# Kernel optimization log

Hardware: AMD Instinct MI355X
Metric: run time of the kernel (lower is better)

## Reference

```python
import jax, jax.numpy as jnp
import numpy as np

B, S, H, NH = 1, 4096, 768, 12
D = H // NH  # per-head dim = 64


def setup_inputs() -> dict:
    key = jax.random.key(0)
    ks = jax.random.split(key, 10)
    p = 0.02  # param scale
    return {
        "x": jax.random.normal(ks[0], (B, S, H), jnp.float32),
        "Wq": jax.random.normal(ks[1], (H, H), jnp.float32) * p,
        "bq": jax.random.normal(ks[2], (H,), jnp.float32) * p,
        "Wk": jax.random.normal(ks[3], (H, H), jnp.float32) * p,
        "bk": jax.random.normal(ks[4], (H,), jnp.float32) * p,
        "Wv": jax.random.normal(ks[5], (H, H), jnp.float32) * p,
        "bv": jax.random.normal(ks[6], (H,), jnp.float32) * p,
        "Wo": jax.random.normal(ks[7], (H, H), jnp.float32) * p,
        "bo": jax.random.normal(ks[8], (H,), jnp.float32) * p,
        "attn_mask": jax.random.randint(ks[9], (B, 1, 1, S), 0, 2).astype(bool),
    }


def _split_heads(t):
    # [B, S, H] -> [B, NH, S, D]
    return t.reshape(B, S, NH, D).transpose(0, 2, 1, 3)


def reference(x, Wq, bq, Wk, bk, Wv, bv, Wo, bo, attn_mask):
    q = _split_heads(x @ Wq.T + bq)
    k = _split_heads(x @ Wk.T + bk)
    v = _split_heads(x @ Wv.T + bv)
    scores = jnp.einsum('bhqd,bhkd->bhqk', q, k) / np.sqrt(D).astype(np.float32)
    scores = jnp.where(attn_mask, jnp.float32(-1e9), scores)
    attn = jax.nn.softmax(scores, axis=-1)
    ctx = jnp.einsum('bhqk,bhkd->bhqd', attn, v)
    ctx = ctx.transpose(0, 2, 1, 3).reshape(B, S, H)  # merge heads
    return ctx @ Wo.T + bo
```

## Files before the change

kernel.cpp:

```cpp
#include <hip/hip_runtime.h>
#include <stdint.h>

#define S_LEN 4096
#define HDIM  768
#define NHEAD 12
#define DHEAD 64

typedef _Float16 f16;
typedef __attribute__((ext_vector_type(8)))  _Float16 f16x8;
typedef __attribute__((ext_vector_type(4)))  _Float16 f16x4;
typedef __attribute__((ext_vector_type(4)))  float    f32x4;
typedef __attribute__((ext_vector_type(16))) float    f32x16;

typedef __attribute__((address_space(1))) void gv_t;
typedef __attribute__((address_space(3))) void lv_t;

__device__ __forceinline__ void async_copy16(const void* g, void* l) {
  __builtin_amdgcn_global_load_lds((gv_t*)g, (lv_t*)l, 16, 0, 0);
}

__device__ __forceinline__ float fast_exp2(float x) {
#if __has_builtin(__builtin_amdgcn_exp2f)
  return __builtin_amdgcn_exp2f(x);
#else
  return exp2f(x);
#endif
}

__device__ __forceinline__ int swz4(int row) { return (row ^ (row >> 2)) & 3; }

constexpr size_t OFF_META = 0;
constexpr size_t OFF_RIDX = 256;
constexpr size_t OFF_XB   = 65536;
constexpr size_t SZ_XB    = (size_t)S_LEN * HDIM * 2;
constexpr size_t OFF_WQKV = OFF_XB + SZ_XB;
constexpr size_t SZ_WQKV  = (size_t)3 * HDIM * HDIM * 2;
constexpr size_t OFF_WO   = OFF_WQKV + SZ_WQKV;
constexpr size_t SZ_WO    = (size_t)HDIM * HDIM * 2;
constexpr size_t OFF_Q    = OFF_WO + SZ_WO;
constexpr size_t SZ_HD    = (size_t)NHEAD * S_LEN * DHEAD * 2;
constexpr size_t OFF_K    = OFF_Q + SZ_HD;
constexpr size_t OFF_VT   = OFF_K + SZ_HD;
constexpr size_t OFF_VR   = OFF_VT + SZ_HD;
constexpr size_t OFF_PO1  = OFF_VR + SZ_HD;

__global__ __launch_bounds__(256) void k_prep(const float* __restrict__ x,
                                              const float* __restrict__ wq,
                                              const float* __restrict__ wk,
                                              const float* __restrict__ wv,
                                              const float* __restrict__ wo,
                                              const int* __restrict__ mi,
                                              f16* __restrict__ dst,
                                              int* __restrict__ ridx,
                                              int* __restrict__ meta) {
  __shared__ int s_flag;
  __shared__ int s_cnt[256];
  const int b = blockIdx.x, tid = threadIdx.x;
  if (b < 5376) {
    int i = b * 256 + tid;
    const float* src; int off;
    if (i < 786432) { src = x; off = i; }
    else {
      int j = i - 786432;
      int w = j / 147456;
      off = j - w * 147456;
      src = (w == 0) ? wq : (w == 1) ? wk : (w == 2) ? wv : wo;
    }
    float4 v = ((const float4*)src)[off];
    f16x4 h;
    h[0] = (f16)v.x; h[1] = (f16)v.y; h[2] = (f16)v.z; h[3] = (f16)v.w;
    ((f16x4*)dst)[i] = h;
    return;
  }
  if (tid == 0) s_flag = 1;
  __syncthreads();
  int bad = 0;
  #pragma unroll
  for (int k = 0; k < 4; ++k) {
    int v = mi[k * 256 + tid];
    if (v != 0 && v != 1) bad = 1;
  }
  if (bad) atomicAnd(&s_flag, 0);
  __syncthreads();
  const int isInt = s_flag;
  const unsigned char* mu8 = (const unsigned char*)mi;
  int keep[16]; int cnt = 0;
  const int s0 = tid * 16;
  #pragma unroll
  for (int k = 0; k < 16; ++k) {
    int mval = isInt ? mi[s0 + k] : (int)mu8[s0 + k];
    keep[k] = (mval == 0) ? 1 : 0;
    cnt += keep[k];
    ridx[s0 + k] = 0;
  }
  s_cnt[tid] = cnt;
  __syncthreads();
  for (int off = 1; off < 256; off <<= 1) {
    int t = (tid >= off) ? s_cnt[tid - off] : 0;
    __syncthreads();
    s_cnt[tid] += t;
    __syncthreads();
  }
  int base = s_cnt[tid] - cnt;
  #pragma unroll
  for (int k = 0; k < 16; ++k) {
    if (keep[k]) { ridx[base] = s0 + k; ++base; }
  }
  if (tid == 255) meta[0] = s_cnt[255];
}

__global__ __launch_bounds__(256) void k_qkv(
    const f16* __restrict__ xb, const f16* __restrict__ wqkv,
    const float* __restrict__ bq, const float* __restrict__ bk, const float* __restrict__ bv,
    const int* __restrict__ ridx, const int* __restrict__ meta,
    f16* __restrict__ Qh, f16* __restrict__ Kc, f16* __restrict__ Vrow) {
  __shared__ __attribute__((aligned(16))) f16 lA[128 * 32];
  __shared__ __attribute__((aligned(16))) f16 lB[128 * 32];
  const int tid = threadIdx.x;
  const int wid = tid >> 6, lane = tid & 63;
  const int hf = lane >> 5, l31 = lane & 31;
  const int wm = wid >> 1, wn = wid & 1;
  const int tn = blockIdx.x;
  const int m0 = blockIdx.y * 128;
  const int mat = tn / 6;
  const int nb = (tn % 6) * 128;
  const int kc = meta[0];
  if (mat != 0 && m0 >= kc) return;
  const f16* wbase = wqkv + (size_t)mat * HDIM * HDIM;

  const int ar0 = tid >> 2, ar1 = 64 + (tid >> 2);
  const f16* asrc0;
  const f16* asrc1;
  if (mat == 0) {
    asrc0 = xb + (size_t)(m0 + ar0) * HDIM;
    asrc1 = xb + (size_t)(m0 + ar1) * HDIM;
  } else {
    int g0 = (m0 + ar0 < kc) ? ridx[m0 + ar0] : 0;
    int g1 = (m0 + ar1 < kc) ? ridx[m0 + ar1] : 0;
    asrc0 = xb + (size_t)g0 * HDIM;
    asrc1 = xb + (size_t)g1 * HDIM;
  }
  const int slot = tid & 3;
  const int gs0 = slot ^ swz4(ar0);
  const int gs1 = slot ^ swz4(ar1);

  f32x16 acc[2][2] = {};

  for (int k0 = 0; k0 < HDIM; k0 += 32) {
    async_copy16((const char*)(asrc0 + k0) + gs0 * 16, (char*)lA + (wid * 64) * 16);
    async_copy16((const char*)(asrc1 + k0) + gs1 * 16, (char*)lA + (256 + wid * 64) * 16);
    async_copy16((const char*)(wbase + (size_t)(nb + ar0) * HDIM + k0) + gs0 * 16,
                 (char*)lB + (wid * 64) * 16);
    async_copy16((const char*)(wbase + (size_t)(nb + ar1) * HDIM + k0) + gs1 * 16,
                 (char*)lB + (256 + wid * 64) * 16);
    __syncthreads();
    #pragma unroll
    for (int kk = 0; kk < 2; ++kk) {
      f16x8 af[2], bf[2];
      #pragma unroll
      for (int mi = 0; mi < 2; ++mi) {
        int row = wm * 64 + mi * 32 + l31;
        af[mi] = *(const f16x8*)&lA[row * 32 + (((kk * 2 + hf) ^ swz4(row)) * 8)];
      }
      #pragma unroll
      for (int ni = 0; ni < 2; ++ni) {
        int row = wn * 64 + ni * 32 + l31;
        bf[ni] = *(const f16x8*)&lB[row * 32 + (((kk * 2 + hf) ^ swz4(row)) * 8)];
      }
      #pragma unroll
      for (int mi = 0; mi < 2; ++mi)
        #pragma unroll
        for (int ni = 0; ni < 2; ++ni)
          acc[mi][ni] = __builtin_amdgcn_mfma_f32_32x32x16_f16(af[mi], bf[ni], acc[mi][ni], 0, 0, 0);
    }
    __syncthreads();
  }

  const float* bias = (mat == 0) ? bq : (mat == 1) ? bk : bv;
  const float qscale = 0.125f * 1.44269504088896341f;
  f16* kvdst = (mat == 1) ? Kc : Vrow;
  #pragma unroll
  for (int mi = 0; mi < 2; ++mi) {
    #pragma unroll
    for (int ni = 0; ni < 2; ++ni) {
      int n = nb + wn * 64 + ni * 32 + l31;
      int head = n >> 6, d = n & 63;
      float b = bias[n];
      #pragma unroll
      for (int reg = 0; reg < 16; ++reg) {
        int s = m0 + wm * 64 + mi * 32 + (reg & 3) + 8 * (reg >> 2) + 4 * hf;
        float val = acc[mi][ni][reg] + b;
        if (mat == 0) {
          Qh[((size_t)head * S_LEN + s) * DHEAD + d] = (f16)(val * qscale);
        } else if (s < kc) {
          kvdst[((size_t)head * S_LEN + s) * DHEAD + d] = (f16)val;
        }
      }
    }
  }
}

__global__ __launch_bounds__(256) void k_vt(const int* __restrict__ meta,
                                            const f16* __restrict__ Vrow,
                                            f16* __restrict__ Vtc,
                                            f16* __restrict__ Kc) {
  const int kc = meta[0];
  const int kcp = (kc + 63) & ~63;
  const int p0 = blockIdx.x * 64;
  const int h = blockIdx.y;
  const int tid = threadIdx.x;
  if (p0 >= kcp) return;
  if (p0 <= kc && kc < p0 + 64 && kc < kcp) {
    const int npad = kcp - kc;
    for (int u = tid; u < npad * 8; u += 256) {
      int r = kc + (u >> 3), c8 = u & 7;
      f16x8 z = {};
      *(f16x8*)&Kc[((size_t)h * S_LEN + r) * DHEAD + c8 * 8] = z;
    }
  }
  __shared__ __attribute__((aligned(16))) f16 lT[64 * 80];
  for (int u = tid; u < 512; u += 256) {
    int d8 = u >> 6, p = u & 63;
    f16x8 v = {};
    if (p0 + p < kc) v = *(const f16x8*)&Vrow[((size_t)h * S_LEN + p0 + p) * DHEAD + d8 * 8];
    #pragma unroll
    for (int j = 0; j < 8; ++j) lT[(d8 * 8 + j) * 80 + p] = v[j];
  }
  __syncthreads();
  for (int w = tid; w < 512; w += 256) {
    int d = w >> 3, p8 = w & 7;
    int base16 = (p8 >> 1) * 16, half = p8 & 1;
    f16x4 lo = *(const f16x4*)&lT[d * 80 + base16 + half * 4];
    f16x4 hi = *(const f16x4*)&lT[d * 80 + base16 + 8 + half * 4];
    f16x8 o;
    o[0] = lo[0]; o[1] = lo[1]; o[2] = lo[2]; o[3] = lo[3];
    o[4] = hi[0]; o[5] = hi[1]; o[6] = hi[2]; o[7] = hi[3];
    *(f16x8*)&Vtc[((size_t)h * DHEAD + d) * S_LEN + p0 + p8 * 8] = o;
  }
}

__global__ __launch_bounds__(256, 3) void k_attn(
    const f16* __restrict__ Qh, const f16* __restrict__ Kc, const f16* __restrict__ Vtc,
    const int* __restrict__ meta, f16* __restrict__ PO0, f16* __restrict__ PO1,
    float* __restrict__ PL) {
  __shared__ __attribute__((aligned(16))) f16 lK[2][64 * 64];
  __shared__ __attribute__((aligned(16))) f16 lV[2][64 * 64];
  const int tid = threadIdx.x;
  const int wid = tid >> 6, lane = tid & 63;
  const int hf = lane >> 5, l31 = lane & 31, r7 = l31 & 7;

  const int lid = blockIdx.x;
  const int w = ((lid & 7) * 96) + (lid >> 3);
  const int head = w >> 6;
  const int rem = w & 63;
  const int split = rem >> 5;
  const int q0 = (rem & 31) * 128 + wid * 32;

  const int kc = meta[0];
  const int nkt = (kc + 63) >> 6;
  const int th = nkt >> 1;
  const int t0 = split ? th : 0;
  const int t1 = split ? nkt : th;

  const f16* Qp = Qh + ((size_t)head * S_LEN + q0 + l31) * DHEAD;
  f16x8 qf[4];
  #pragma unroll
  for (int dc = 0; dc < 4; ++dc) qf[dc] = *(const f16x8*)(Qp + dc * 16 + hf * 8);

  f32x16 accO[2] = {};
  float ls0 = 0.f, ls1 = 0.f, ls2 = 0.f, ls3 = 0.f;

  const char* kbase = (const char*)(Kc + (size_t)head * S_LEN * DHEAD);
  const char* vbase = (const char*)(Vtc + (size_t)head * DHEAD * S_LEN);

  const int c0row = tid >> 3,         c0slot = tid & 7;
  const int c1row = (256 + tid) >> 3, c1slot = tid & 7;
  const int gs0 = c0slot ^ (c0row & 7);
  const int gs1 = c1slot ^ (c1row & 7);

  auto stage = [&](int t, int buf) {
    const int j0 = t * 64;
    async_copy16(kbase + (size_t)(j0 + c0row) * 128 + gs0 * 16,
                 (char*)&lK[buf][0] + (wid * 64) * 16);
    async_copy16(vbase + (size_t)c0row * (S_LEN * 2) + (size_t)j0 * 2 + gs0 * 16,
                 (char*)&lV[buf][0] + (wid * 64) * 16);
    async_copy16(kbase + (size_t)(j0 + c1row) * 128 + gs1 * 16,
                 (char*)&lK[buf][0] + (256 + wid * 64) * 16);
    async_copy16(vbase + (size_t)c1row * (S_LEN * 2) + (size_t)j0 * 2 + gs1 * 16,
                 (char*)&lV[buf][0] + (256 + wid * 64) * 16);
  };

  int cur = 0;
  if (t0 < t1) {
    stage(t0, 0);
    __syncthreads();
  }

  for (int t = t0; t < t1; ++t) {
    const bool more = (t + 1 < t1);
    if (more) stage(t + 1, cur ^ 1);

    #pragma unroll
    for (int mh = 0; mh < 2; ++mh) {
      f16x8 af[4];
      const int arow = mh * 32 + l31;
      #pragma unroll
      for (int dc = 0; dc < 4; ++dc)
        af[dc] = *(const f16x8*)&lK[cur][arow * 64 + ((((dc << 1) | hf) ^ r7) * 8)];
      f32x16 s = {};
      #pragma unroll
      for (int dc = 0; dc < 4; ++dc)
        s = __builtin_amdgcn_mfma_f32_32x32x16_f16(af[dc], qf[dc], s, 0, 0, 0);
      #pragma unroll
      for (int u = 0; u < 16; ++u) {
        s[u] = fast_exp2(s[u]);
        if ((u & 3) == 0) ls0 += s[u];
        else if ((u & 3) == 1) ls1 += s[u];
        else if ((u & 3) == 2) ls2 += s[u];
        else ls3 += s[u];
      }
      #pragma unroll
      for (int cc = 0; cc < 2; ++cc) {
        f16x8 pf;
        #pragma unroll
        for (int u = 0; u < 8; ++u) pf[u] = (f16)s[8 * cc + u];
        const int c2 = mh * 2 + cc;
        #pragma unroll
        for (int dh = 0; dh < 2; ++dh) {
          const int vrow = dh * 32 + l31;
          f16x8 vf = *(const f16x8*)&lV[cur][vrow * 64 + ((((c2 << 1) | hf) ^ r7) * 8)];
          accO[dh] = __builtin_amdgcn_mfma_f32_32x32x16_f16(pf, vf, accO[dh], 0, 0, 0);
        }
      }
    }

    if (more) {
      __syncthreads();
      cur ^= 1;
    }
  }

  float lsum = (ls0 + ls1) + (ls2 + ls3);
  lsum += __shfl_xor(lsum, 32);
  if (split == 1) lsum -= (float)(nkt * 64 - kc);
  if (hf == 0)
    PL[((size_t)split * NHEAD + head) * S_LEN + q0 + l31] = lsum;

  __syncthreads();
  f16* ost = (f16*)lK;
  #pragma unroll
  for (int dh = 0; dh < 2; ++dh)
    #pragma unroll
    for (int reg = 0; reg < 16; ++reg) {
      int row = (reg & 3) + 8 * (reg >> 2) + 4 * hf;
      ost[wid * 2048 + row * 64 + dh * 32 + l31] = (f16)accO[dh][reg];
    }
  f16* PO = split ? PO1 : PO0;
  const f16* osrc = ost + wid * 2048;
  #pragma unroll
  for (int p = 0; p < 4; ++p) {
    int row = p * 8 + (lane >> 3), sl = lane & 7;
    f16x8 v = *(const f16x8*)&osrc[row * 64 + sl * 8];
    *(f16x8*)&PO[((size_t)head * S_LEN + q0 + row) * DHEAD + sl * 8] = v;
  }
}

__global__ __launch_bounds__(256) void k_out(
    const f16* __restrict__ PO0, const f16* __restrict__ PO1,
    const float* __restrict__ PL, const f16* __restrict__ wo,
    const float* __restrict__ bo, float* __restrict__ out) {
  __shared__ __attribute__((aligned(16))) f16 lA[128 * 64];
  __shared__ __attribute__((aligned(16))) f16 lB[64 * 64];
  __shared__ float linv[NHEAD * 128];
  const int tid = threadIdx.x;
  const int wid = tid >> 6, lane = tid & 63;
  const int hf = lane >> 5, l31 = lane & 31;
  const int wm = wid >> 1, wn = wid & 1;
  const int lid = blockIdx.x;
  const int w = ((lid & 7) * 48) + (lid >> 3);
  const int nb = (w % 12) * 64;
  const int m0 = (w / 12) * 128;

  for (int i = tid; i < NHEAD * 128; i += 256) {
    int h = i >> 7, r = i & 127;
    float l = PL[(size_t)h * S_LEN + m0 + r] + PL[(size_t)(NHEAD + h) * S_LEN + m0 + r];
    linv[i] = 1.0f / l;
  }
  __syncthreads();

  f32x16 acc[2] = {};

  for (int head = 0; head < NHEAD; ++head) {
    #pragma unroll
    for (int it = 0; it < 4; ++it) {
      int c = it * 256 + tid;
      int row = c >> 3, slot = c & 7;
      int gs = slot ^ (row & 7);
      size_t pi = ((size_t)head * S_LEN + m0 + row) * DHEAD + gs * 8;
      f16x8 a0 = *(const f16x8*)(PO0 + pi);
      f16x8 a1 = *(const f16x8*)(PO1 + pi);
      float il = linv[head * 128 + row];
      f16x8 av;
      #pragma unroll
      for (int u = 0; u < 8; ++u) av[u] = (f16)(((float)a0[u] + (float)a1[u]) * il);
      *(f16x8*)&lA[c * 8] = av;
    }
    #pragma unroll
    for (int it = 0; it < 2; ++it) {
      int c = it * 256 + tid;
      int row = c >> 3, slot = c & 7;
      int gs = slot ^ (row & 7);
      async_copy16((const char*)(wo + (size_t)(nb + row) * HDIM + head * 64) + gs * 16,
                   (char*)lB + (it * 256 + wid * 64) * 16);
    }
    __syncthreads();
    #pragma unroll
    for (int kk = 0; kk < 4; ++kk) {
      f16x8 af[2], bf;
      #pragma unroll
      for (int mi = 0; mi < 2; ++mi) {
        int row = wm * 64 + mi * 32 + l31;
        af[mi] = *(const f16x8*)&lA[row * 64 + ((((kk << 1) | hf) ^ (row & 7)) * 8)];
      }
      int rb = wn * 32 + l31;
      bf = *(const f16x8*)&lB[rb * 64 + ((((kk << 1) | hf) ^ (rb & 7)) * 8)];
      #pragma unroll
      for (int mi = 0; mi < 2; ++mi)
        acc[mi] = __builtin_amdgcn_mfma_f32_32x32x16_f16(af[mi], bf, acc[mi], 0, 0, 0);
    }
    __syncthreads();
  }

  const int n = nb + wn * 32 + l31;
  const float b = bo[n];
  #pragma unroll
  for (int mi = 0; mi < 2; ++mi) {
    #pragma unroll
    for (int reg = 0; reg < 16; ++reg) {
      int s = m0 + wm * 64 + mi * 32 + (reg & 3) + 8 * (reg >> 2) + 4 * hf;
      out[(size_t)s * HDIM + n] = acc[mi][reg] + b;
    }
  }
}

extern "C" void kernel_launch(void* const* d_in, const int* in_sizes, int n_in,
                              void* d_out, int out_size, void* d_ws, size_t ws_size,
                              hipStream_t stream) {
  const float* x  = (const float*)d_in[0];
  const float* Wq = (const float*)d_in[1];
  const float* bq = (const float*)d_in[2];
  const float* Wk = (const float*)d_in[3];
  const float* bk = (const float*)d_in[4];
  const float* Wv = (const float*)d_in[5];
  const float* bv = (const float*)d_in[6];
  const float* Wo = (const float*)d_in[7];
  const float* bo = (const float*)d_in[8];
  const int*   mask = (const int*)d_in[9];
  float* out = (float*)d_out;

  char* ws = (char*)d_ws;
  int* meta  = (int*)(ws + OFF_META);
  int* ridx  = (int*)(ws + OFF_RIDX);
  f16* xb    = (f16*)(ws + OFF_XB);
  f16* wqkv  = (f16*)(ws + OFF_WQKV);
  f16* wob   = (f16*)(ws + OFF_WO);
  f16* Qh    = (f16*)(ws + OFF_Q);
  f16* Kc    = (f16*)(ws + OFF_K);
  f16* Vtc   = (f16*)(ws + OFF_VT);
  f16* Vrow  = (f16*)(ws + OFF_VR);
  f16* PO0   = (f16*)(ws + OFF_VR);
  f16* PO1   = (f16*)(ws + OFF_PO1);
  float* PL  = (float*)(ws + OFF_WQKV);

  k_prep<<<dim3(5377), 256, 0, stream>>>(x, Wq, Wk, Wv, Wo, mask, xb, ridx, meta);
  k_qkv<<<dim3(18, 32), 256, 0, stream>>>(xb, wqkv, bq, bk, bv, ridx, meta, Qh, Kc, Vrow);
  k_vt<<<dim3(64, NHEAD), 256, 0, stream>>>(meta, Vrow, Vtc, Kc);
  k_attn<<<dim3(768), 256, 0, stream>>>(Qh, Kc, Vtc, meta, PO0, PO1, PL);
  k_out<<<dim3(384), 256, 0, stream>>>(PO0, PO1, PL, wob, bo, out);
}
```

Before: 175.9 us.

## Widen QKV GEMM K-tile to 64 and interleave attention MFMA chains with setprio

The QKV projection GEMM now stages 64-wide K slices instead of 32, using an 8-slot XOR swizzle. This halves the number of barrier pairs per output tile at the cost of twice the LDS per block. The attention inner loop now computes both 32-row key halves' score MFMAs together as two independent chains. The exp/sum and P·V MFMAs are batched and interleaved, and s_setprio is raised around the MFMA bursts. This exposes more instruction-level parallelism and helps overlap with other waves, but increases register pressure.

```diff
diff --git a/kernel.cpp b/kernel.cpp
--- a/kernel.cpp
+++ b/kernel.cpp
@@ -114,8 +114,8 @@
     const float* __restrict__ bq, const float* __restrict__ bk, const float* __restrict__ bv,
     const int* __restrict__ ridx, const int* __restrict__ meta,
     f16* __restrict__ Qh, f16* __restrict__ Kc, f16* __restrict__ Vrow) {
-  __shared__ __attribute__((aligned(16))) f16 lA[128 * 32];
-  __shared__ __attribute__((aligned(16))) f16 lB[128 * 32];
+  __shared__ __attribute__((aligned(16))) f16 lA[128 * 64];
+  __shared__ __attribute__((aligned(16))) f16 lB[128 * 64];
   const int tid = threadIdx.x;
   const int wid = tid >> 6, lane = tid & 63;
   const int hf = lane >> 5, l31 = lane & 31;
@@ -128,44 +128,45 @@
   if (mat != 0 && m0 >= kc) return;
   const f16* wbase = wqkv + (size_t)mat * HDIM * HDIM;
 
-  const int ar0 = tid >> 2, ar1 = 64 + (tid >> 2);
-  const f16* asrc0;
-  const f16* asrc1;
-  if (mat == 0) {
-    asrc0 = xb + (size_t)(m0 + ar0) * HDIM;
-    asrc1 = xb + (size_t)(m0 + ar1) * HDIM;
-  } else {
-    int g0 = (m0 + ar0 < kc) ? ridx[m0 + ar0] : 0;
-    int g1 = (m0 + ar1 < kc) ? ridx[m0 + ar1] : 0;
-    asrc0 = xb + (size_t)g0 * HDIM;
-    asrc1 = xb + (size_t)g1 * HDIM;
-  }
-  const int slot = tid & 3;
-  const int gs0 = slot ^ swz4(ar0);
-  const int gs1 = slot ^ swz4(ar1);
+  const int r8 = tid >> 3;
+  const int slot = tid & 7;
+  const int gs = slot ^ (r8 & 7);
+  const f16* asrc[4];
+  #pragma unroll
+  for (int it = 0; it < 4; ++it) {
+    int r = it * 32 + r8;
+    if (mat == 0) {
+      asrc[it] = xb + (size_t)(m0 + r) * HDIM;
+    } else {
+      int g = (m0 + r < kc) ? ridx[m0 + r] : 0;
+      asrc[it] = xb + (size_t)g * HDIM;
+    }
+  }
 
   f32x16 acc[2][2] = {};
 
-  for (int k0 = 0; k0 < HDIM; k0 += 32) {
-    async_copy16((const char*)(asrc0 + k0) + gs0 * 16, (char*)lA + (wid * 64) * 16);
-    async_copy16((const char*)(asrc1 + k0) + gs1 * 16, (char*)lA + (256 + wid * 64) * 16);
-    async_copy16((const char*)(wbase + (size_t)(nb + ar0) * HDIM + k0) + gs0 * 16,
-                 (char*)lB + (wid * 64) * 16);
-    async_copy16((const char*)(wbase + (size_t)(nb + ar1) * HDIM + k0) + gs1 * 16,
-                 (char*)lB + (256 + wid * 64) * 16);
-    __syncthreads();
-    #pragma unroll
-    for (int kk = 0; kk < 2; ++kk) {
+  for (int k0 = 0; k0 < HDIM; k0 += 64) {
+    #pragma unroll
+    for (int it = 0; it < 4; ++it) {
+      int r = it * 32 + r8;
+      async_copy16((const char*)(asrc[it] + k0) + gs * 16,
+                   (char*)lA + (it * 256 + wid * 64) * 16);
+      async_copy16((const char*)(wbase + (size_t)(nb + r) * HDIM + k0) + gs * 16,
+                   (char*)lB + (it * 256 + wid * 64) * 16);
+    }
+    __syncthreads();
+    #pragma unroll
+    for (int kk = 0; kk < 4; ++kk) {
       f16x8 af[2], bf[2];
       #pragma unroll
       for (int mi = 0; mi < 2; ++mi) {
         int row = wm * 64 + mi * 32 + l31;
-        af[mi] = *(const f16x8*)&lA[row * 32 + (((kk * 2 + hf) ^ swz4(row)) * 8)];
+        af[mi] = *(const f16x8*)&lA[row * 64 + ((((kk << 1) | hf) ^ (row & 7)) * 8)];
       }
       #pragma unroll
       for (int ni = 0; ni < 2; ++ni) {
         int row = wn * 64 + ni * 32 + l31;
-        bf[ni] = *(const f16x8*)&lB[row * 32 + (((kk * 2 + hf) ^ swz4(row)) * 8)];
+        bf[ni] = *(const f16x8*)&lB[row * 64 + ((((kk << 1) | hf) ^ (row & 7)) * 8)];
       }
       #pragma unroll
       for (int mi = 0; mi < 2; ++mi)
@@ -300,39 +301,50 @@
     const bool more = (t + 1 < t1);
     if (more) stage(t + 1, cur ^ 1);
 
-    #pragma unroll
-    for (int mh = 0; mh < 2; ++mh) {
-      f16x8 af[4];
-      const int arow = mh * 32 + l31;
-      #pragma unroll
-      for (int dc = 0; dc < 4; ++dc)
-        af[dc] = *(const f16x8*)&lK[cur][arow * 64 + ((((dc << 1) | hf) ^ r7) * 8)];
-      f32x16 s = {};
-      #pragma unroll
-      for (int dc = 0; dc < 4; ++dc)
-        s = __builtin_amdgcn_mfma_f32_32x32x16_f16(af[dc], qf[dc], s, 0, 0, 0);
-      #pragma unroll
-      for (int u = 0; u < 16; ++u) {
-        s[u] = fast_exp2(s[u]);
-        if ((u & 3) == 0) ls0 += s[u];
-        else if ((u & 3) == 1) ls1 += s[u];
-        else if ((u & 3) == 2) ls2 += s[u];
-        else ls3 += s[u];
-      }
-      #pragma unroll
-      for (int cc = 0; cc < 2; ++cc) {
-        f16x8 pf;
-        #pragma unroll
-        for (int u = 0; u < 8; ++u) pf[u] = (f16)s[8 * cc + u];
-        const int c2 = mh * 2 + cc;
-        #pragma unroll
-        for (int dh = 0; dh < 2; ++dh) {
-          const int vrow = dh * 32 + l31;
-          f16x8 vf = *(const f16x8*)&lV[cur][vrow * 64 + ((((c2 << 1) | hf) ^ r7) * 8)];
-          accO[dh] = __builtin_amdgcn_mfma_f32_32x32x16_f16(pf, vf, accO[dh], 0, 0, 0);
-        }
-      }
-    }
+    f16x8 af0[4], af1[4];
+    #pragma unroll
+    for (int dc = 0; dc < 4; ++dc) {
+      af0[dc] = *(const f16x8*)&lK[cur][l31 * 64 + ((((dc << 1) | hf) ^ r7) * 8)];
+      af1[dc] = *(const f16x8*)&lK[cur][(32 + l31) * 64 + ((((dc << 1) | hf) ^ r7) * 8)];
+    }
+    f32x16 sA = {}, sB = {};
+    __builtin_amdgcn_s_setprio(1);
+    #pragma unroll
+    for (int dc = 0; dc < 4; ++dc) {
+      sA = __builtin_amdgcn_mfma_f32_32x32x16_f16(af0[dc], qf[dc], sA, 0, 0, 0);
+      sB = __builtin_amdgcn_mfma_f32_32x32x16_f16(af1[dc], qf[dc], sB, 0, 0, 0);
+    }
+    __builtin_amdgcn_s_setprio(0);
+
+    f16x8 pf0[2], pf1[2];
+    #pragma unroll
+    for (int u = 0; u < 16; ++u) {
+      sA[u] = fast_exp2(sA[u]);
+      sB[u] = fast_exp2(sB[u]);
+      if (u & 1) { ls1 += sA[u]; ls3 += sB[u]; }
+      else       { ls0 += sA[u]; ls2 += sB[u]; }
+    }
+    #pragma unroll
+    for (int cc = 0; cc < 2; ++cc)
+      #pragma unroll
+      for (int u = 0; u < 8; ++u) {
+        pf0[cc][u] = (f16)sA[8 * cc + u];
+        pf1[cc][u] = (f16)sB[8 * cc + u];
+      }
+
+    __builtin_amdgcn_s_setprio(1);
+    #pragma unroll
+    for (int cc = 0; cc < 2; ++cc) {
+      #pragma unroll
+      for (int dh = 0; dh < 2; ++dh) {
+        const int vrow = dh * 32 + l31;
+        f16x8 vf0 = *(const f16x8*)&lV[cur][vrow * 64 + ((((cc << 1) | hf) ^ r7) * 8)];
+        f16x8 vf1 = *(const f16x8*)&lV[cur][vrow * 64 + (((((2 + cc) << 1) | hf) ^ r7) * 8)];
+        accO[dh] = __builtin_amdgcn_mfma_f32_32x32x16_f16(pf0[cc], vf0, accO[dh], 0, 0, 0);
+        accO[dh] = __builtin_amdgcn_mfma_f32_32x32x16_f16(pf1[cc], vf1, accO[dh], 0, 0, 0);
+      }
+    }
+    __builtin_amdgcn_s_setprio(0);
 
     if (more) {
       __syncthreads();
```

New measurement: 182.3 us. 3.7% more time.

## Software-pipeline QK^T of next tile with softmax and PV of current tile

Applied to the files above, without the earlier changes.

The attention inner loop is restructured so the score MFMAs for the next K tile run while exp2 and the P·V MFMAs for the current tile are issued. This is meant to hide the MFMA-to-exp dependency and keep the matrix units busy. K/V shared buffers go from double to triple buffering so the tile two steps ahead can be staged. In exchange, LDS per block grows by half and register pressure rises from the extra live score accumulators, which may hurt occupancy at the 3-blocks-per-CU launch bound.

```diff
diff --git a/kernel.cpp b/kernel.cpp
--- a/kernel.cpp
+++ b/kernel.cpp
@@ -243,8 +243,8 @@
     const f16* __restrict__ Qh, const f16* __restrict__ Kc, const f16* __restrict__ Vtc,
     const int* __restrict__ meta, f16* __restrict__ PO0, f16* __restrict__ PO1,
     float* __restrict__ PL) {
-  __shared__ __attribute__((aligned(16))) f16 lK[2][64 * 64];
-  __shared__ __attribute__((aligned(16))) f16 lV[2][64 * 64];
+  __shared__ __attribute__((aligned(16))) f16 lK[3][64 * 64];
+  __shared__ __attribute__((aligned(16))) f16 lV[3][64 * 64];
   const int tid = threadIdx.x;
   const int wid = tid >> 6, lane = tid & 63;
   const int hf = lane >> 5, l31 = lane & 31, r7 = l31 & 7;
@@ -291,53 +291,79 @@
   };
 
   int cur = 0;
+  f32x16 sA = {}, sB = {};
   if (t0 < t1) {
     stage(t0, 0);
-    __syncthreads();
+    if (t0 + 1 < t1) stage(t0 + 1, 1);
+    __syncthreads();
+    f16x8 a0[4], a1[4];
+    #pragma unroll
+    for (int dc = 0; dc < 4; ++dc) {
+      a0[dc] = *(const f16x8*)&lK[0][l31 * 64 + ((((dc << 1) | hf) ^ r7) * 8)];
+      a1[dc] = *(const f16x8*)&lK[0][(32 + l31) * 64 + ((((dc << 1) | hf) ^ r7) * 8)];
+    }
+    #pragma unroll
+    for (int dc = 0; dc < 4; ++dc) {
+      sA = __builtin_amdgcn_mfma_f32_32x32x16_f16(a0[dc], qf[dc], sA, 0, 0, 0);
+      sB = __builtin_amdgcn_mfma_f32_32x32x16_f16(a1[dc], qf[dc], sB, 0, 0, 0);
+    }
   }
 
   for (int t = t0; t < t1; ++t) {
+    const int nxt = (cur == 2) ? 0 : cur + 1;
+    const int nn  = (nxt == 2) ? 0 : nxt + 1;
     const bool more = (t + 1 < t1);
-    if (more) stage(t + 1, cur ^ 1);
-
-    #pragma unroll
-    for (int mh = 0; mh < 2; ++mh) {
-      f16x8 af[4];
-      const int arow = mh * 32 + l31;
-      #pragma unroll
-      for (int dc = 0; dc < 4; ++dc)
-        af[dc] = *(const f16x8*)&lK[cur][arow * 64 + ((((dc << 1) | hf) ^ r7) * 8)];
-      f32x16 s = {};
-      #pragma unroll
-      for (int dc = 0; dc < 4; ++dc)
-        s = __builtin_amdgcn_mfma_f32_32x32x16_f16(af[dc], qf[dc], s, 0, 0, 0);
-      #pragma unroll
-      for (int u = 0; u < 16; ++u) {
-        s[u] = fast_exp2(s[u]);
-        if ((u & 3) == 0) ls0 += s[u];
-        else if ((u & 3) == 1) ls1 += s[u];
-        else if ((u & 3) == 2) ls2 += s[u];
-        else ls3 += s[u];
-      }
-      #pragma unroll
-      for (int cc = 0; cc < 2; ++cc) {
-        f16x8 pf;
-        #pragma unroll
-        for (int u = 0; u < 8; ++u) pf[u] = (f16)s[8 * cc + u];
-        const int c2 = mh * 2 + cc;
-        #pragma unroll
-        for (int dh = 0; dh < 2; ++dh) {
-          const int vrow = dh * 32 + l31;
-          f16x8 vf = *(const f16x8*)&lV[cur][vrow * 64 + ((((c2 << 1) | hf) ^ r7) * 8)];
-          accO[dh] = __builtin_amdgcn_mfma_f32_32x32x16_f16(pf, vf, accO[dh], 0, 0, 0);
-        }
-      }
-    }
-
+    if (t + 2 < t1) stage(t + 2, nn);
+
+    f16x8 a0[4], a1[4];
     if (more) {
-      __syncthreads();
-      cur ^= 1;
-    }
+      #pragma unroll
+      for (int dc = 0; dc < 4; ++dc) {
+        a0[dc] = *(const f16x8*)&lK[nxt][l31 * 64 + ((((dc << 1) | hf) ^ r7) * 8)];
+        a1[dc] = *(const f16x8*)&lK[nxt][(32 + l31) * 64 + ((((dc << 1) | hf) ^ r7) * 8)];
+      }
+    }
+
+    f16x8 pf0[2], pf1[2];
+    #pragma unroll
+    for (int u = 0; u < 16; ++u) {
+      sA[u] = fast_exp2(sA[u]);
+      sB[u] = fast_exp2(sB[u]);
+      if (u & 1) { ls1 += sA[u]; ls3 += sB[u]; }
+      else       { ls0 += sA[u]; ls2 += sB[u]; }
+    }
+    #pragma unroll
+    for (int cc = 0; cc < 2; ++cc)
+      #pragma unroll
+      for (int u = 0; u < 8; ++u) {
+        pf0[cc][u] = (f16)sA[8 * cc + u];
+        pf1[cc][u] = (f16)sB[8 * cc + u];
+      }
+
+    f32x16 s2A = {}, s2B = {};
+    if (more) {
+      #pragma unroll
+      for (int dc = 0; dc < 4; ++dc) {
+        s2A = __builtin_amdgcn_mfma_f32_32x32x16_f16(a0[dc], qf[dc], s2A, 0, 0, 0);
+        s2B = __builtin_amdgcn_mfma_f32_32x32x16_f16(a1[dc], qf[dc], s2B, 0, 0, 0);
+      }
+    }
+
+    #pragma unroll
+    for (int cc = 0; cc < 2; ++cc) {
+      #pragma unroll
+      for (int dh = 0; dh < 2; ++dh) {
+        const int vrow = dh * 32 + l31;
+        f16x8 vf0 = *(const f16x8*)&lV[cur][vrow * 64 + ((((cc << 1) | hf) ^ r7) * 8)];
+        f16x8 vf1 = *(const f16x8*)&lV[cur][vrow * 64 + (((((2 + cc) << 1) | hf) ^ r7) * 8)];
+        accO[dh] = __builtin_amdgcn_mfma_f32_32x32x16_f16(pf0[cc], vf0, accO[dh], 0, 0, 0);
+        accO[dh] = __builtin_amdgcn_mfma_f32_32x32x16_f16(pf1[cc], vf1, accO[dh], 0, 0, 0);
+      }
+    }
+
+    if (more) __syncthreads();
+    sA = s2A; sB = s2B;
+    cur = nxt;
   }
 
   float lsum = (ls0 + ls1) + (ls2 + ls3);
```

New measurement: 203.4 us. 1.16x slower.

## Process two 32-row query blocks per wave in attention to reuse K/V tiles

Applied to the files above, without the earlier changes.

Each wave now handles 64 query rows as two 32-row blocks, so every K and V fragment loaded from LDS feeds two MFMAs, and each block covers 256 queries. The grid halves to 384 blocks, which halves total K/V global-to-LDS staging traffic. In exchange, register pressure rises (double accumulators and Q fragments), so the occupancy hint drops from 3 to 2 blocks per CU, and with fewer blocks there is less parallelism to hide latency.

```diff
diff --git a/kernel.cpp b/kernel.cpp
--- a/kernel.cpp
+++ b/kernel.cpp
@@ -239,22 +239,21 @@
   }
 }
 
-__global__ __launch_bounds__(256, 3) void k_attn(
+__global__ __launch_bounds__(256, 2) void k_attn(
     const f16* __restrict__ Qh, const f16* __restrict__ Kc, const f16* __restrict__ Vtc,
     const int* __restrict__ meta, f16* __restrict__ PO0, f16* __restrict__ PO1,
     float* __restrict__ PL) {
-  __shared__ __attribute__((aligned(16))) f16 lK[2][64 * 64];
-  __shared__ __attribute__((aligned(16))) f16 lV[2][64 * 64];
+  __shared__ __attribute__((aligned(16))) f16 lKV[4][64 * 64];
   const int tid = threadIdx.x;
   const int wid = tid >> 6, lane = tid & 63;
   const int hf = lane >> 5, l31 = lane & 31, r7 = l31 & 7;
 
   const int lid = blockIdx.x;
-  const int w = ((lid & 7) * 96) + (lid >> 3);
-  const int head = w >> 6;
-  const int rem = w & 63;
-  const int split = rem >> 5;
-  const int q0 = (rem & 31) * 128 + wid * 32;
+  const int w = ((lid & 7) * 48) + (lid >> 3);
+  const int head = w >> 5;
+  const int rem = w & 31;
+  const int split = rem >> 4;
+  const int qw = (rem & 15) * 256 + wid * 64;
 
   const int kc = meta[0];
   const int nkt = (kc + 63) >> 6;
@@ -262,13 +261,16 @@
   const int t0 = split ? th : 0;
   const int t1 = split ? nkt : th;
 
-  const f16* Qp = Qh + ((size_t)head * S_LEN + q0 + l31) * DHEAD;
-  f16x8 qf[4];
-  #pragma unroll
-  for (int dc = 0; dc < 4; ++dc) qf[dc] = *(const f16x8*)(Qp + dc * 16 + hf * 8);
-
-  f32x16 accO[2] = {};
-  float ls0 = 0.f, ls1 = 0.f, ls2 = 0.f, ls3 = 0.f;
+  f16x8 qf[2][4];
+  #pragma unroll
+  for (int qb = 0; qb < 2; ++qb) {
+    const f16* Qp = Qh + ((size_t)head * S_LEN + qw + qb * 32 + l31) * DHEAD;
+    #pragma unroll
+    for (int dc = 0; dc < 4; ++dc) qf[qb][dc] = *(const f16x8*)(Qp + dc * 16 + hf * 8);
+  }
+
+  f32x16 accO[2][2] = {};
+  float ls[2][2] = {};
 
   const char* kbase = (const char*)(Kc + (size_t)head * S_LEN * DHEAD);
   const char* vbase = (const char*)(Vtc + (size_t)head * DHEAD * S_LEN);
@@ -281,13 +283,13 @@
   auto stage = [&](int t, int buf) {
     const int j0 = t * 64;
     async_copy16(kbase + (size_t)(j0 + c0row) * 128 + gs0 * 16,
-                 (char*)&lK[buf][0] + (wid * 64) * 16);
+                 (char*)&lKV[buf][0] + (wid * 64) * 16);
     async_copy16(vbase + (size_t)c0row * (S_LEN * 2) + (size_t)j0 * 2 + gs0 * 16,
-                 (char*)&lV[buf][0] + (wid * 64) * 16);
+                 (char*)&lKV[2 + buf][0] + (wid * 64) * 16);
     async_copy16(kbase + (size_t)(j0 + c1row) * 128 + gs1 * 16,
-                 (char*)&lK[buf][0] + (256 + wid * 64) * 16);
+                 (char*)&lKV[buf][0] + (256 + wid * 64) * 16);
     async_copy16(vbase + (size_t)c1row * (S_LEN * 2) + (size_t)j0 * 2 + gs1 * 16,
-                 (char*)&lV[buf][0] + (256 + wid * 64) * 16);
+                 (char*)&lKV[2 + buf][0] + (256 + wid * 64) * 16);
   };
 
   int cur = 0;
@@ -306,30 +308,34 @@
       const int arow = mh * 32 + l31;
       #pragma unroll
       for (int dc = 0; dc < 4; ++dc)
-        af[dc] = *(const f16x8*)&lK[cur][arow * 64 + ((((dc << 1) | hf) ^ r7) * 8)];
-      f32x16 s = {};
-      #pragma unroll
-      for (int dc = 0; dc < 4; ++dc)
-        s = __builtin_amdgcn_mfma_f32_32x32x16_f16(af[dc], qf[dc], s, 0, 0, 0);
-      #pragma unroll
-      for (int u = 0; u < 16; ++u) {
-        s[u] = fast_exp2(s[u]);
-        if ((u & 3) == 0) ls0 += s[u];
-        else if ((u & 3) == 1) ls1 += s[u];
-        else if ((u & 3) == 2) ls2 += s[u];
-        else ls3 += s[u];
+        af[dc] = *(const f16x8*)&lKV[cur][arow * 64 + ((((dc << 1) | hf) ^ r7) * 8)];
+
+      f16x8 pf[2][2];
+      #pragma unroll
+      for (int qb = 0; qb < 2; ++qb) {
+        f32x16 s = {};
+        #pragma unroll
+        for (int dc = 0; dc < 4; ++dc)
+          s = __builtin_amdgcn_mfma_f32_32x32x16_f16(af[dc], qf[qb][dc], s, 0, 0, 0);
+        #pragma unroll
+        for (int u = 0; u < 16; ++u) {
+          s[u] = fast_exp2(s[u]);
+          ls[qb][u & 1] += s[u];
+        }
+        #pragma unroll
+        for (int cc = 0; cc < 2; ++cc)
+          #pragma unroll
+          for (int u = 0; u < 8; ++u) pf[qb][cc][u] = (f16)s[8 * cc + u];
       }
       #pragma unroll
       for (int cc = 0; cc < 2; ++cc) {
-        f16x8 pf;
-        #pragma unroll
-        for (int u = 0; u < 8; ++u) pf[u] = (f16)s[8 * cc + u];
         const int c2 = mh * 2 + cc;
         #pragma unroll
         for (int dh = 0; dh < 2; ++dh) {
           const int vrow = dh * 32 + l31;
-          f16x8 vf = *(const f16x8*)&lV[cur][vrow * 64 + ((((c2 << 1) | hf) ^ r7) * 8)];
-          accO[dh] = __builtin_amdgcn_mfma_f32_32x32x16_f16(pf, vf, accO[dh], 0, 0, 0);
+          f16x8 vf = *(const f16x8*)&lKV[2 + cur][vrow * 64 + ((((c2 << 1) | hf) ^ r7) * 8)];
+          accO[0][dh] = __builtin_amdgcn_mfma_f32_32x32x16_f16(pf[0][cc], vf, accO[0][dh], 0, 0, 0);
+          accO[1][dh] = __builtin_amdgcn_mfma_f32_32x32x16_f16(pf[1][cc], vf, accO[1][dh], 0, 0, 0);
         }
       }
     }
@@ -340,28 +346,29 @@
     }
   }
 
-  float lsum = (ls0 + ls1) + (ls2 + ls3);
-  lsum += __shfl_xor(lsum, 32);
-  if (split == 1) lsum -= (float)(nkt * 64 - kc);
-  if (hf == 0)
-    PL[((size_t)split * NHEAD + head) * S_LEN + q0 + l31] = lsum;
-
-  __syncthreads();
-  f16* ost = (f16*)lK;
-  #pragma unroll
-  for (int dh = 0; dh < 2; ++dh)
-    #pragma unroll
-    for (int reg = 0; reg < 16; ++reg) {
-      int row = (reg & 3) + 8 * (reg >> 2) + 4 * hf;
-      ost[wid * 2048 + row * 64 + dh * 32 + l31] = (f16)accO[dh][reg];
-    }
   f16* PO = split ? PO1 : PO0;
-  const f16* osrc = ost + wid * 2048;
-  #pragma unroll
-  for (int p = 0; p < 4; ++p) {
+  __syncthreads();
+  f16* ost = (f16*)lKV + wid * 4096;
+  #pragma unroll
+  for (int qb = 0; qb < 2; ++qb) {
+    float lsum = ls[qb][0] + ls[qb][1];
+    lsum += __shfl_xor(lsum, 32);
+    if (split == 1) lsum -= (float)(nkt * 64 - kc);
+    if (hf == 0)
+      PL[((size_t)split * NHEAD + head) * S_LEN + qw + qb * 32 + l31] = lsum;
+    #pragma unroll
+    for (int dh = 0; dh < 2; ++dh)
+      #pragma unroll
+      for (int reg = 0; reg < 16; ++reg) {
+        int row = qb * 32 + (reg & 3) + 8 * (reg >> 2) + 4 * hf;
+        ost[row * 64 + dh * 32 + l31] = (f16)accO[qb][dh][reg];
+      }
+  }
+  #pragma unroll
+  for (int p = 0; p < 8; ++p) {
     int row = p * 8 + (lane >> 3), sl = lane & 7;
-    f16x8 v = *(const f16x8*)&osrc[row * 64 + sl * 8];
-    *(f16x8*)&PO[((size_t)head * S_LEN + q0 + row) * DHEAD + sl * 8] = v;
+    f16x8 v = *(const f16x8*)&ost[row * 64 + sl * 8];
+    *(f16x8*)&PO[((size_t)head * S_LEN + qw + row) * DHEAD + sl * 8] = v;
   }
 }
 
@@ -475,6 +482,6 @@
   k_prep<<<dim3(5377), 256, 0, stream>>>(x, Wq, Wk, Wv, Wo, mask, xb, ridx, meta);
   k_qkv<<<dim3(18, 32), 256, 0, stream>>>(xb, wqkv, bq, bk, bv, ridx, meta, Qh, Kc, Vrow);
   k_vt<<<dim3(64, NHEAD), 256, 0, stream>>>(meta, Vrow, Vtc, Kc);
-  k_attn<<<dim3(768), 256, 0, stream>>>(Qh, Kc, Vtc, meta, PO0, PO1, PL);
+  k_attn<<<dim3(384), 256, 0, stream>>>(Qh, Kc, Vtc, meta, PO0, PO1, PL);
   k_out<<<dim3(384), 256, 0, stream>>>(PO0, PO1, PL, wob, bo, out);
 }
```

After: 177.2 us. No clear change (+0.7%).
